# Optimization experiments

Hardware: AMD Instinct MI355X
Metric: run time of the kernel (lower is better)

## Reference

```python
import jax, jax.numpy as jnp
import numpy as np

K_NEIGHBORS = 5
EPS = 1e-12  # torch F.normalize eps


def _l2_normalize(x):
    n = jnp.linalg.norm(x, axis=-1, keepdims=True)
    return x / jnp.maximum(n, EPS)


def setup_inputs() -> dict:
    key = jax.random.key(0)
    k1, k2, k3, k4 = jax.random.split(key, 4)
    B, D = 256, 512
    N, A = 50000, 8
    return {
        "z_flowed": jax.random.normal(k1, (B, D), dtype=jnp.float32),
        "target_attrs": jax.random.randint(k2, (B, A), 0, 3, dtype=jnp.int32),
        "train_embeddings": jax.random.normal(k3, (N, D), dtype=jnp.float32),
        "train_attributes": jax.random.randint(k4, (N, A), 0, 3, dtype=jnp.int32),
    }


def reference(z_flowed, target_attrs, train_embeddings, train_attributes):
    B = z_flowed.shape[0]
    A = target_attrs.shape[1]
    z_norm = _l2_normalize(z_flowed)          # [B, D]
    train_norm = _l2_normalize(train_embeddings)  # [N, D]

    # batched attribute match: [B, N] count of matching attributes
    match_score = (train_attributes[None, :, :] == target_attrs[:, None, :]).sum(-1)
    mask = (match_score >= (A - 1)).astype(z_norm.dtype)  # [B, N]

    # cosine similarities for all samples in one GEMM: [B, N]
    sims = jnp.einsum('nd,bd->bn', train_norm, z_norm)
    masked_sim = sims * mask

    top_k_values, _ = jax.lax.top_k(masked_sim, K_NEIGHBORS)  # [B, K]
    per_sample_loss = (1.0 - top_k_values).mean(-1)           # [B]

    # samples with fewer than k matching neighbors are skipped in the sum
    valid = (mask.sum(-1) >= K_NEIGHBORS).astype(per_sample_loss.dtype)
    return (per_sample_loss * valid).sum() / B
```

## Files before the change

kernel.cpp:

```cpp
#include <hip/hip_runtime.h>
#include <math.h>


constexpr int D = 512;
constexpr int A = 8;
constexpr int K_NEI = 5;
constexpr int SLOTS = 512;
constexpr int CSTRIDE = 16;
constexpr int PAIR_CAP = 65536;
constexpr int LDS_PAIR_CAP = 1024;

__device__ __forceinline__ float wave_reduce_add(float v) {
    #pragma unroll
    for (int m = 1; m < 64; m <<= 1) v += __shfl_xor(v, m, 64);
    return v;
}

__global__ __launch_bounds__(64) void prep_kernel(
    const float* __restrict__ z, const int* __restrict__ tattr,
    float* __restrict__ z_norm, unsigned* __restrict__ tpacked,
    int* __restrict__ counters, int* __restrict__ npairs,
    float* __restrict__ out)
{
    const int b = blockIdx.x;
    const int lane = threadIdx.x;
    const float4* zrow = (const float4*)(z + (size_t)b * D);
    float4 v0 = zrow[lane * 2 + 0];
    float4 v1 = zrow[lane * 2 + 1];
    float ss = v0.x*v0.x + v0.y*v0.y + v0.z*v0.z + v0.w*v0.w
             + v1.x*v1.x + v1.y*v1.y + v1.z*v1.z + v1.w*v1.w;
    ss = wave_reduce_add(ss);
    const float scale = 1.0f / fmaxf(sqrtf(ss), 1e-12f);
    v0.x *= scale; v0.y *= scale; v0.z *= scale; v0.w *= scale;
    v1.x *= scale; v1.y *= scale; v1.z *= scale; v1.w *= scale;
    float4* orow = (float4*)(z_norm + (size_t)b * D);
    orow[lane * 2 + 0] = v0;
    orow[lane * 2 + 1] = v1;
    if (lane == 0) {
        unsigned p = 0;
        #pragma unroll
        for (int a = 0; a < A; a++)
            p |= ((unsigned)tattr[b * A + a] & 0xFu) << (4 * a);
        tpacked[b] = p;
        counters[b * CSTRIDE] = 0;
        if (b == 0) { *npairs = 0; out[0] = 0.0f; }
    }
}

__global__ __launch_bounds__(256) void match_kernel(
    const int* __restrict__ trattr, const unsigned* __restrict__ tpacked,
    unsigned* __restrict__ pairs, int* __restrict__ npairs, int N)
{
    __shared__ unsigned s_tp[256];
    __shared__ unsigned s_pairs[LDS_PAIR_CAP];
    __shared__ int s_cnt, s_base;

    const int tid = threadIdx.x;
    const int n = blockIdx.x * 256 + tid;
    s_tp[tid] = tpacked[tid];
    if (tid == 0) s_cnt = 0;
    __syncthreads();

    unsigned p = 0;
    if (n < N) {
        const int4* a4 = (const int4*)(trattr + (size_t)n * A);
        const int4 x = a4[0], y = a4[1];
        p  = ((unsigned)x.x & 0xFu)       | (((unsigned)x.y & 0xFu) << 4)
           | (((unsigned)x.z & 0xFu) << 8)  | (((unsigned)x.w & 0xFu) << 12)
           | (((unsigned)y.x & 0xFu) << 16) | (((unsigned)y.y & 0xFu) << 20)
           | (((unsigned)y.z & 0xFu) << 24) | (((unsigned)y.w & 0xFu) << 28);
    }

    if (n < N) {
        const uint4* tp4 = (const uint4*)s_tp;
        #pragma unroll 4
        for (int bq = 0; bq < 64; bq++) {
            const uint4 t = tp4[bq];
            #pragma unroll
            for (int j = 0; j < 4; j++) {
                const unsigned tv = (j == 0) ? t.x : (j == 1) ? t.y : (j == 2) ? t.z : t.w;
                const unsigned yv = p ^ tv;
                const unsigned nzhi = ((((yv & 0x77777777u) + 0x77777777u) | yv) & 0x88888888u);
                if (__popc(nzhi) <= 1) {
                    const int idx = atomicAdd(&s_cnt, 1);
                    const unsigned pr = ((unsigned)n << 8) | (unsigned)(bq * 4 + j);
                    if (idx < LDS_PAIR_CAP) s_pairs[idx] = pr;
                }
            }
        }
    }
    __syncthreads();
    const int cnt = min(s_cnt, LDS_PAIR_CAP);
    if (tid == 0) s_base = atomicAdd(npairs, cnt);
    __syncthreads();
    const int base = s_base;
    for (int i = tid; i < cnt; i += 256)
        if (base + i < PAIR_CAP) pairs[base + i] = s_pairs[i];
}

__global__ __launch_bounds__(256) void dot_kernel(
    const float* __restrict__ train, const float* __restrict__ z_norm,
    const unsigned* __restrict__ pairs, const int* __restrict__ npairs,
    int* __restrict__ counters, float* __restrict__ simbuf)
{
    const int lane = threadIdx.x & 63;
    const int w = blockIdx.x * 4 + (threadIdx.x >> 6);
    const int nwaves = gridDim.x * 4;
    const int np = min(*npairs, PAIR_CAP);

    for (int i = w; i < np; i += nwaves) {
        const unsigned pr = pairs[i];
        const int n = (int)(pr >> 8);
        const int b = (int)(pr & 255u);
        const float4* row4 = (const float4*)(train + (size_t)n * D);
        const float4* zr4  = (const float4*)(z_norm + (size_t)b * D);
        const float4 r0 = row4[lane * 2 + 0];
        const float4 r1 = row4[lane * 2 + 1];
        const float4 z0 = zr4[lane * 2 + 0];
        const float4 z1 = zr4[lane * 2 + 1];
        float ss = r0.x*r0.x + r0.y*r0.y + r0.z*r0.z + r0.w*r0.w
                 + r1.x*r1.x + r1.y*r1.y + r1.z*r1.z + r1.w*r1.w;
        float dd = r0.x*z0.x + r0.y*z0.y + r0.z*z0.z + r0.w*z0.w
                 + r1.x*z1.x + r1.y*z1.y + r1.z*z1.z + r1.w*z1.w;
        #pragma unroll
        for (int m = 1; m < 64; m <<= 1) {
            ss += __shfl_xor(ss, m, 64);
            dd += __shfl_xor(dd, m, 64);
        }
        if (lane == 0) {
            const float sim = dd / fmaxf(sqrtf(ss), 1e-12f);
            const int idx = atomicAdd(&counters[b * CSTRIDE], 1);
            if (idx < SLOTS) simbuf[(size_t)b * SLOTS + idx] = sim;
        }
    }
}

__global__ __launch_bounds__(64) void topk_kernel(
    const int* __restrict__ counters, const float* __restrict__ simbuf,
    float* __restrict__ out, int Bt)
{
    const int b = blockIdx.x;
    const int lane = threadIdx.x;
    const int cnt = counters[b * CSTRIDE];
    const int m = min(cnt, SLOTS);
    const float* buf = simbuf + (size_t)b * SLOTS;

    float v[8];
    #pragma unroll
    for (int k = 0; k < 8; k++) {
        const int i = lane + k * 64;
        v[k] = (i < m) ? buf[i] : -1e30f;
    }

    float s = 0.0f;
    #pragma unroll
    for (int r = 0; r < K_NEI; r++) {
        float best = v[0];
        #pragma unroll
        for (int k = 1; k < 8; k++) best = fmaxf(best, v[k]);
        float M = best;
        #pragma unroll
        for (int mm = 1; mm < 64; mm <<= 1) M = fmaxf(M, __shfl_xor(M, mm, 64));
        s += fmaxf(M, 0.0f);
        const unsigned long long bal = __ballot(best == M);
        const int first = __ffsll(bal) - 1;
        if (lane == first) {
            if      (v[0] == M) v[0] = -1e30f;
            else if (v[1] == M) v[1] = -1e30f;
            else if (v[2] == M) v[2] = -1e30f;
            else if (v[3] == M) v[3] = -1e30f;
            else if (v[4] == M) v[4] = -1e30f;
            else if (v[5] == M) v[5] = -1e30f;
            else if (v[6] == M) v[6] = -1e30f;
            else                v[7] = -1e30f;
        }
    }

    if (lane == 0) {
        const float contrib = (cnt >= K_NEI) ? (1.0f - s * (1.0f / K_NEI)) : 0.0f;
        atomicAdd(out, contrib / (float)Bt);
    }
}

extern "C" void kernel_launch(void* const* d_in, const int* in_sizes, int n_in,
                              void* d_out, int out_size, void* d_ws, size_t ws_size,
                              hipStream_t stream)
{
    const float* z      = (const float*)d_in[0];
    const int*   tattr  = (const int*)d_in[1];
    const float* train  = (const float*)d_in[2];
    const int*   trattr = (const int*)d_in[3];
    float* out = (float*)d_out;

    const int B = in_sizes[0] / D;
    const int N = in_sizes[2] / D;

    char* ws = (char*)d_ws;
    float*    z_norm   = (float*)ws;   ws += (size_t)B * D * sizeof(float);
    unsigned* tpacked  = (unsigned*)ws; ws += (size_t)B * sizeof(unsigned);
    int*      counters = (int*)ws;     ws += (size_t)B * CSTRIDE * sizeof(int);
    float*    simbuf   = (float*)ws;   ws += (size_t)B * SLOTS * sizeof(float);
    int*      npairs   = (int*)ws;     ws += 64;
    unsigned* pairs    = (unsigned*)ws;

    prep_kernel<<<B, 64, 0, stream>>>(z, tattr, z_norm, tpacked, counters, npairs, out);
    match_kernel<<<(N + 255) / 256, 256, 0, stream>>>(trattr, tpacked, pairs, npairs, N);
    dot_kernel<<<1024, 256, 0, stream>>>(train, z_norm, pairs, npairs, counters, simbuf);
    topk_kernel<<<B, 64, 0, stream>>>(counters, simbuf, out, B);
}
```

Baseline: 181.4 us.

## Fuse attribute matching and dot-product stages into one kernel using LDS pair list

Merges the match and dot kernels so that each block computes the cosine similarities for its own matched pairs straight from shared memory. This removes the global pair buffer, the global pair counter atomic and one kernel launch. In exchange, the dot work is confined to the 4 waves of the block that found the pairs, so it can be unevenly spread. The LDS pair capacity is doubled so fewer overflow drops occur.

```diff
diff --git a/kernel.cpp b/kernel.cpp
--- a/kernel.cpp
+++ b/kernel.cpp
@@ -7,8 +7,7 @@
 constexpr int K_NEI = 5;
 constexpr int SLOTS = 512;
 constexpr int CSTRIDE = 16;
-constexpr int PAIR_CAP = 65536;
-constexpr int LDS_PAIR_CAP = 1024;
+constexpr int LDS_PAIR_CAP = 2048;
 
 __device__ __forceinline__ float wave_reduce_add(float v) {
     #pragma unroll
@@ -19,8 +18,7 @@
 __global__ __launch_bounds__(64) void prep_kernel(
     const float* __restrict__ z, const int* __restrict__ tattr,
     float* __restrict__ z_norm, unsigned* __restrict__ tpacked,
-    int* __restrict__ counters, int* __restrict__ npairs,
-    float* __restrict__ out)
+    int* __restrict__ counters, float* __restrict__ out)
 {
     const int b = blockIdx.x;
     const int lane = threadIdx.x;
@@ -43,17 +41,18 @@
             p |= ((unsigned)tattr[b * A + a] & 0xFu) << (4 * a);
         tpacked[b] = p;
         counters[b * CSTRIDE] = 0;
-        if (b == 0) { *npairs = 0; out[0] = 0.0f; }
+        if (b == 0) out[0] = 0.0f;
     }
 }
 
-__global__ __launch_bounds__(256) void match_kernel(
+__global__ __launch_bounds__(256) void match_dot_kernel(
     const int* __restrict__ trattr, const unsigned* __restrict__ tpacked,
-    unsigned* __restrict__ pairs, int* __restrict__ npairs, int N)
+    const float* __restrict__ train, const float* __restrict__ z_norm,
+    int* __restrict__ counters, float* __restrict__ simbuf, int N)
 {
     __shared__ unsigned s_tp[256];
     __shared__ unsigned s_pairs[LDS_PAIR_CAP];
-    __shared__ int s_cnt, s_base;
+    __shared__ int s_cnt;
 
     const int tid = threadIdx.x;
     const int n = blockIdx.x * 256 + tid;
@@ -61,17 +60,15 @@
     if (tid == 0) s_cnt = 0;
     __syncthreads();
 
-    unsigned p = 0;
     if (n < N) {
         const int4* a4 = (const int4*)(trattr + (size_t)n * A);
         const int4 x = a4[0], y = a4[1];
-        p  = ((unsigned)x.x & 0xFu)       | (((unsigned)x.y & 0xFu) << 4)
+        const unsigned p =
+             ((unsigned)x.x & 0xFu)        | (((unsigned)x.y & 0xFu) << 4)
            | (((unsigned)x.z & 0xFu) << 8)  | (((unsigned)x.w & 0xFu) << 12)
            | (((unsigned)y.x & 0xFu) << 16) | (((unsigned)y.y & 0xFu) << 20)
            | (((unsigned)y.z & 0xFu) << 24) | (((unsigned)y.w & 0xFu) << 28);
-    }
 
-    if (n < N) {
         const uint4* tp4 = (const uint4*)s_tp;
         #pragma unroll 4
         for (int bq = 0; bq < 64; bq++) {
@@ -83,36 +80,22 @@
                 const unsigned nzhi = ((((yv & 0x77777777u) + 0x77777777u) | yv) & 0x88888888u);
                 if (__popc(nzhi) <= 1) {
                     const int idx = atomicAdd(&s_cnt, 1);
-                    const unsigned pr = ((unsigned)n << 8) | (unsigned)(bq * 4 + j);
-                    if (idx < LDS_PAIR_CAP) s_pairs[idx] = pr;
+                    if (idx < LDS_PAIR_CAP)
+                        s_pairs[idx] = ((unsigned)n << 8) | (unsigned)(bq * 4 + j);
                 }
             }
         }
     }
     __syncthreads();
+
     const int cnt = min(s_cnt, LDS_PAIR_CAP);
-    if (tid == 0) s_base = atomicAdd(npairs, cnt);
-    __syncthreads();
-    const int base = s_base;
-    for (int i = tid; i < cnt; i += 256)
-        if (base + i < PAIR_CAP) pairs[base + i] = s_pairs[i];
-}
-
-__global__ __launch_bounds__(256) void dot_kernel(
-    const float* __restrict__ train, const float* __restrict__ z_norm,
-    const unsigned* __restrict__ pairs, const int* __restrict__ npairs,
-    int* __restrict__ counters, float* __restrict__ simbuf)
-{
-    const int lane = threadIdx.x & 63;
-    const int w = blockIdx.x * 4 + (threadIdx.x >> 6);
-    const int nwaves = gridDim.x * 4;
-    const int np = min(*npairs, PAIR_CAP);
-
-    for (int i = w; i < np; i += nwaves) {
-        const unsigned pr = pairs[i];
-        const int n = (int)(pr >> 8);
-        const int b = (int)(pr & 255u);
-        const float4* row4 = (const float4*)(train + (size_t)n * D);
+    const int lane = tid & 63;
+    const int w = tid >> 6;
+    for (int i = w; i < cnt; i += 4) {
+        const unsigned pr = s_pairs[i];
+        const int nn = (int)(pr >> 8);
+        const int b  = (int)(pr & 255u);
+        const float4* row4 = (const float4*)(train + (size_t)nn * D);
         const float4* zr4  = (const float4*)(z_norm + (size_t)b * D);
         const float4 r0 = row4[lane * 2 + 0];
         const float4 r1 = row4[lane * 2 + 1];
@@ -196,15 +179,13 @@
     const int N = in_sizes[2] / D;
 
     char* ws = (char*)d_ws;
-    float*    z_norm   = (float*)ws;   ws += (size_t)B * D * sizeof(float);
+    float*    z_norm   = (float*)ws;    ws += (size_t)B * D * sizeof(float);
     unsigned* tpacked  = (unsigned*)ws; ws += (size_t)B * sizeof(unsigned);
-    int*      counters = (int*)ws;     ws += (size_t)B * CSTRIDE * sizeof(int);
-    float*    simbuf   = (float*)ws;   ws += (size_t)B * SLOTS * sizeof(float);
-    int*      npairs   = (int*)ws;     ws += 64;
-    unsigned* pairs    = (unsigned*)ws;
+    int*      counters = (int*)ws;      ws += (size_t)B * CSTRIDE * sizeof(int);
+    float*    simbuf   = (float*)ws;
 
-    prep_kernel<<<B, 64, 0, stream>>>(z, tattr, z_norm, tpacked, counters, npairs, out);
-    match_kernel<<<(N + 255) / 256, 256, 0, stream>>>(trattr, tpacked, pairs, npairs, N);
-    dot_kernel<<<1024, 256, 0, stream>>>(train, z_norm, pairs, npairs, counters, simbuf);
+    prep_kernel<<<B, 64, 0, stream>>>(z, tattr, z_norm, tpacked, counters, out);
+    match_dot_kernel<<<(N + 255) / 256, 256, 0, stream>>>(
+        trattr, tpacked, train, z_norm, counters, simbuf, N);
     topk_kernel<<<B, 64, 0, stream>>>(counters, simbuf, out, B);
 }
```

Result: slower. 220.9 us (+21.8%).

## Replace global atomic slotting with per-block histogram scan and quarter-wave dot products

Applied to the files above, without the earlier changes.

Match kernel now builds a per-block per-query histogram and ranks, a serial scan kernel computes offsets, and the dot kernel writes similarities to deterministic slots instead of using global atomics on per-query counters. The dot kernel processes four pairs per wave using 16-lane groups, with more blocks. The final sum uses a separate reduction kernel instead of atomicAdd. This adds two launches and a serial 196-step scan over 256 columns, which may cost more than the global atomics it removes.

```diff
diff --git a/kernel.cpp b/kernel.cpp
--- a/kernel.cpp
+++ b/kernel.cpp
@@ -6,9 +6,9 @@
 constexpr int A = 8;
 constexpr int K_NEI = 5;
 constexpr int SLOTS = 512;
-constexpr int CSTRIDE = 16;
 constexpr int PAIR_CAP = 65536;
-constexpr int LDS_PAIR_CAP = 1024;
+constexpr int LDS_PAIR_CAP = 512;
+constexpr int DOT_BLOCKS = 2048;
 
 __device__ __forceinline__ float wave_reduce_add(float v) {
     #pragma unroll
@@ -17,10 +17,8 @@
 }
 
 __global__ __launch_bounds__(64) void prep_kernel(
-    const float* __restrict__ z, const int* __restrict__ tattr,
-    float* __restrict__ z_norm, unsigned* __restrict__ tpacked,
-    int* __restrict__ counters, int* __restrict__ npairs,
-    float* __restrict__ out)
+    const float* __restrict__ z, float* __restrict__ z_norm,
+    int* __restrict__ npairs)
 {
     const int b = blockIdx.x;
     const int lane = threadIdx.x;
@@ -36,42 +34,43 @@
     float4* orow = (float4*)(z_norm + (size_t)b * D);
     orow[lane * 2 + 0] = v0;
     orow[lane * 2 + 1] = v1;
-    if (lane == 0) {
-        unsigned p = 0;
-        #pragma unroll
-        for (int a = 0; a < A; a++)
-            p |= ((unsigned)tattr[b * A + a] & 0xFu) << (4 * a);
-        tpacked[b] = p;
-        counters[b * CSTRIDE] = 0;
-        if (b == 0) { *npairs = 0; out[0] = 0.0f; }
-    }
+    if (b == 0 && lane == 0) *npairs = 0;
 }
 
 __global__ __launch_bounds__(256) void match_kernel(
-    const int* __restrict__ trattr, const unsigned* __restrict__ tpacked,
-    unsigned* __restrict__ pairs, int* __restrict__ npairs, int N)
+    const int* __restrict__ trattr, const int* __restrict__ tattr,
+    unsigned* __restrict__ pairs, int* __restrict__ npairs,
+    int* __restrict__ h, int N)
 {
     __shared__ unsigned s_tp[256];
     __shared__ unsigned s_pairs[LDS_PAIR_CAP];
+    __shared__ int s_hist[256];
     __shared__ int s_cnt, s_base;
 
     const int tid = threadIdx.x;
     const int n = blockIdx.x * 256 + tid;
-    s_tp[tid] = tpacked[tid];
+
+    {
+        const int4* t4 = (const int4*)(tattr + (size_t)tid * A);
+        const int4 x = t4[0], y = t4[1];
+        s_tp[tid] = ((unsigned)x.x & 0xFu)        | (((unsigned)x.y & 0xFu) << 4)
+                  | (((unsigned)x.z & 0xFu) << 8)  | (((unsigned)x.w & 0xFu) << 12)
+                  | (((unsigned)y.x & 0xFu) << 16) | (((unsigned)y.y & 0xFu) << 20)
+                  | (((unsigned)y.z & 0xFu) << 24) | (((unsigned)y.w & 0xFu) << 28);
+    }
+    s_hist[tid] = 0;
     if (tid == 0) s_cnt = 0;
     __syncthreads();
 
-    unsigned p = 0;
     if (n < N) {
         const int4* a4 = (const int4*)(trattr + (size_t)n * A);
         const int4 x = a4[0], y = a4[1];
-        p  = ((unsigned)x.x & 0xFu)       | (((unsigned)x.y & 0xFu) << 4)
+        const unsigned p =
+             ((unsigned)x.x & 0xFu)        | (((unsigned)x.y & 0xFu) << 4)
            | (((unsigned)x.z & 0xFu) << 8)  | (((unsigned)x.w & 0xFu) << 12)
            | (((unsigned)y.x & 0xFu) << 16) | (((unsigned)y.y & 0xFu) << 20)
            | (((unsigned)y.z & 0xFu) << 24) | (((unsigned)y.w & 0xFu) << 28);
-    }
-
-    if (n < N) {
+
         const uint4* tp4 = (const uint4*)s_tp;
         #pragma unroll 4
         for (int bq = 0; bq < 64; bq++) {
@@ -82,14 +81,20 @@
                 const unsigned yv = p ^ tv;
                 const unsigned nzhi = ((((yv & 0x77777777u) + 0x77777777u) | yv) & 0x88888888u);
                 if (__popc(nzhi) <= 1) {
-                    const int idx = atomicAdd(&s_cnt, 1);
-                    const unsigned pr = ((unsigned)n << 8) | (unsigned)(bq * 4 + j);
-                    if (idx < LDS_PAIR_CAP) s_pairs[idx] = pr;
+                    const int b = bq * 4 + j;
+                    const int rank = atomicAdd(&s_hist[b], 1);
+                    const int idx  = atomicAdd(&s_cnt, 1);
+                    if (idx < LDS_PAIR_CAP && rank < 256)
+                        s_pairs[idx] = ((unsigned)n << 16) | ((unsigned)rank << 8)
+                                     | (unsigned)b;
                 }
             }
         }
     }
     __syncthreads();
+
+    h[blockIdx.x * 256 + tid] = s_hist[tid];
+
     const int cnt = min(s_cnt, LDS_PAIR_CAP);
     if (tid == 0) s_base = atomicAdd(npairs, cnt);
     __syncthreads();
@@ -98,52 +103,78 @@
         if (base + i < PAIR_CAP) pairs[base + i] = s_pairs[i];
 }
 
+__global__ __launch_bounds__(256) void scan_kernel(
+    const int* __restrict__ h, int* __restrict__ offs,
+    int* __restrict__ cntb, int NBLK)
+{
+    const int b = threadIdx.x;
+    int run = 0;
+    for (int blk = 0; blk < NBLK; blk++) {
+        const int v = h[blk * 256 + b];
+        offs[blk * 256 + b] = run;
+        run += v;
+    }
+    cntb[b] = run;
+}
+
 __global__ __launch_bounds__(256) void dot_kernel(
     const float* __restrict__ train, const float* __restrict__ z_norm,
     const unsigned* __restrict__ pairs, const int* __restrict__ npairs,
-    int* __restrict__ counters, float* __restrict__ simbuf)
-{
-    const int lane = threadIdx.x & 63;
-    const int w = blockIdx.x * 4 + (threadIdx.x >> 6);
-    const int nwaves = gridDim.x * 4;
+    const int* __restrict__ offs, float* __restrict__ sims)
+{
     const int np = min(*npairs, PAIR_CAP);
-
-    for (int i = w; i < np; i += nwaves) {
-        const unsigned pr = pairs[i];
-        const int n = (int)(pr >> 8);
-        const int b = (int)(pr & 255u);
-        const float4* row4 = (const float4*)(train + (size_t)n * D);
-        const float4* zr4  = (const float4*)(z_norm + (size_t)b * D);
-        const float4 r0 = row4[lane * 2 + 0];
-        const float4 r1 = row4[lane * 2 + 1];
-        const float4 z0 = zr4[lane * 2 + 0];
-        const float4 z1 = zr4[lane * 2 + 1];
-        float ss = r0.x*r0.x + r0.y*r0.y + r0.z*r0.z + r0.w*r0.w
-                 + r1.x*r1.x + r1.y*r1.y + r1.z*r1.z + r1.w*r1.w;
-        float dd = r0.x*z0.x + r0.y*z0.y + r0.z*z0.z + r0.w*z0.w
-                 + r1.x*z1.x + r1.y*z1.y + r1.z*z1.z + r1.w*z1.w;
+    const int tid = threadIdx.x;
+    const int lane = tid & 63;
+    const int q  = lane >> 4;
+    const int ql = lane & 15;
+    const int w = blockIdx.x * 4 + (tid >> 6);
+    const int stride = DOT_BLOCKS * 4 * 4;
+
+    for (int p0 = w * 4; p0 < np; p0 += stride) {
+        const int idx = p0 + q;
+        const bool active = (idx < np);
+        unsigned pr = 0;
+        float ss = 0.0f, dd = 0.0f;
+        if (active) {
+            pr = pairs[idx];
+            const int n = (int)(pr >> 16);
+            const int b = (int)(pr & 255u);
+            const float4* r4 = (const float4*)(train  + (size_t)n * D);
+            const float4* z4 = (const float4*)(z_norm + (size_t)b * D);
+            #pragma unroll
+            for (int j = 0; j < 8; j++) {
+                const float4 r  = r4[j * 16 + ql];
+                const float4 zz = z4[j * 16 + ql];
+                ss += r.x*r.x  + r.y*r.y  + r.z*r.z  + r.w*r.w;
+                dd += r.x*zz.x + r.y*zz.y + r.z*zz.z + r.w*zz.w;
+            }
+        }
         #pragma unroll
-        for (int m = 1; m < 64; m <<= 1) {
+        for (int m = 1; m < 16; m <<= 1) {
             ss += __shfl_xor(ss, m, 64);
             dd += __shfl_xor(dd, m, 64);
         }
-        if (lane == 0) {
-            const float sim = dd / fmaxf(sqrtf(ss), 1e-12f);
-            const int idx = atomicAdd(&counters[b * CSTRIDE], 1);
-            if (idx < SLOTS) simbuf[(size_t)b * SLOTS + idx] = sim;
+        if (active && ql == 0) {
+            const int n    = (int)(pr >> 16);
+            const int b    = (int)(pr & 255u);
+            const int rank = (int)((pr >> 8) & 255u);
+            const int blk  = n >> 8;
+            const int dest = offs[blk * 256 + b] + rank;
+            if (dest < SLOTS)
+                sims[(size_t)b * SLOTS + dest] = dd / fmaxf(sqrtf(ss), 1e-12f);
         }
     }
 }
 
 __global__ __launch_bounds__(64) void topk_kernel(
-    const int* __restrict__ counters, const float* __restrict__ simbuf,
-    float* __restrict__ out, int Bt)
+    const int* __restrict__ cntb, const float* __restrict__ sims,
+    float* __restrict__ contrib, int Bt)
 {
     const int b = blockIdx.x;
     const int lane = threadIdx.x;
-    const int cnt = counters[b * CSTRIDE];
+    const int cnt = cntb[b];
     const int m = min(cnt, SLOTS);
-    const float* buf = simbuf + (size_t)b * SLOTS;
+    const float* buf = sims + (size_t)b * SLOTS;
 
     float v[8];
     #pragma unroll
@@ -176,10 +207,17 @@
         }
     }
 
-    if (lane == 0) {
-        const float contrib = (cnt >= K_NEI) ? (1.0f - s * (1.0f / K_NEI)) : 0.0f;
-        atomicAdd(out, contrib / (float)Bt);
-    }
+    if (lane == 0)
+        contrib[b] = (cnt >= K_NEI) ? (1.0f - s * (1.0f / K_NEI)) / (float)Bt : 0.0f;
+}
+
+__global__ __launch_bounds__(64) void final_kernel(
+    const float* __restrict__ contrib, float* __restrict__ out, int Bt)
+{
+    float s = 0.0f;
+    for (int i = threadIdx.x; i < Bt; i += 64) s += contrib[i];
+    s = wave_reduce_add(s);
+    if (threadIdx.x == 0) out[0] = s;
 }
 
 extern "C" void kernel_launch(void* const* d_in, const int* in_sizes, int n_in,
@@ -194,17 +232,22 @@
 
     const int B = in_sizes[0] / D;
     const int N = in_sizes[2] / D;
+    const int NBLK = (N + 255) / 256;
 
     char* ws = (char*)d_ws;
-    float*    z_norm   = (float*)ws;   ws += (size_t)B * D * sizeof(float);
-    unsigned* tpacked  = (unsigned*)ws; ws += (size_t)B * sizeof(unsigned);
-    int*      counters = (int*)ws;     ws += (size_t)B * CSTRIDE * sizeof(int);
-    float*    simbuf   = (float*)ws;   ws += (size_t)B * SLOTS * sizeof(float);
-    int*      npairs   = (int*)ws;     ws += 64;
-    unsigned* pairs    = (unsigned*)ws;
-
-    prep_kernel<<<B, 64, 0, stream>>>(z, tattr, z_norm, tpacked, counters, npairs, out);
-    match_kernel<<<(N + 255) / 256, 256, 0, stream>>>(trattr, tpacked, pairs, npairs, N);
-    dot_kernel<<<1024, 256, 0, stream>>>(train, z_norm, pairs, npairs, counters, simbuf);
-    topk_kernel<<<B, 64, 0, stream>>>(counters, simbuf, out, B);
-}
+    float*    z_norm  = (float*)ws;    ws += (size_t)B * D * sizeof(float);
+    int*      h       = (int*)ws;      ws += (size_t)NBLK * 256 * sizeof(int);
+    int*      offs    = (int*)ws;      ws += (size_t)NBLK * 256 * sizeof(int);
+    int*      cntb    = (int*)ws;      ws += (size_t)B * sizeof(int);
+    int*      npairs  = (int*)ws;      ws += 64;
+    unsigned* pairs   = (unsigned*)ws; ws += (size_t)PAIR_CAP * sizeof(unsigned);
+    float*    sims    = (float*)ws;    ws += (size_t)B * SLOTS * sizeof(float);
+    float*    contrib = (float*)ws;
+
+    prep_kernel<<<B, 64, 0, stream>>>(z, z_norm, npairs);
+    match_kernel<<<NBLK, 256, 0, stream>>>(trattr, tattr, pairs, npairs, h, N);
+    scan_kernel<<<1, 256, 0, stream>>>(h, offs, cntb, NBLK);
+    dot_kernel<<<DOT_BLOCKS, 256, 0, stream>>>(train, z_norm, pairs, npairs, offs, sims);
+    topk_kernel<<<B, 64, 0, stream>>>(cntb, sims, contrib, B);
+    final_kernel<<<1, 64, 0, stream>>>(contrib, out, B);
+}
```

Result: slower. 226.5 us (+24.8%).
